# Optimization experiments

Hardware: AMD Instinct MI355X
Metric: run time of the kernel (lower is better)

The kernel has to match this reference:

```python
import jax, jax.numpy as jnp
import numpy as np

E, EDIM, NDIM, H = 262144, 256, 256, 8
DH = NDIM // H
EPS = 1e-5  # torch nn.LayerNorm default


def _param(k, shape, scale=0.02):
    return jax.random.normal(k, shape, jnp.float32) * scale


def setup_inputs() -> dict:
    key = jax.random.key(0)
    ks = jax.random.split(key, 12)
    return {
        "x": jax.random.normal(ks[0], (E, EDIM), jnp.float32),
        "src_x": jax.random.normal(ks[1], (E, NDIM), jnp.float32),
        "dst_x": jax.random.normal(ks[2], (E, NDIM), jnp.float32),
        # multi-head cross-attention params (q from edge feats, k/v from node feats)
        "Wq": _param(ks[3], (EDIM, NDIM)), "bq": jnp.zeros((NDIM,), jnp.float32),
        "Wk": _param(ks[4], (NDIM, NDIM)), "bk": jnp.zeros((NDIM,), jnp.float32),
        "Wv": _param(ks[5], (NDIM, NDIM)), "bv": jnp.zeros((NDIM,), jnp.float32),
        "Wo": _param(ks[6], (NDIM, EDIM)), "bo": jnp.zeros((EDIM,), jnp.float32),
        "W1": _param(ks[7], (EDIM, 4 * EDIM)), "b1": jnp.zeros((4 * EDIM,), jnp.float32),
        "W2": _param(ks[8], (4 * EDIM, EDIM)), "b2": jnp.zeros((EDIM,), jnp.float32),
        # two LayerNorms
        "g1": jnp.ones((EDIM,), jnp.float32), "be1": jnp.zeros((EDIM,), jnp.float32),
        "g2": jnp.ones((EDIM,), jnp.float32), "be2": jnp.zeros((EDIM,), jnp.float32),
    }


def _layer_norm(h, g, b):
    m = jnp.mean(h, axis=-1, keepdims=True)
    v = jnp.mean(jnp.square(h - m), axis=-1, keepdims=True)
    return (h - m) * jax.lax.rsqrt(v + EPS) * g + b


def reference(x, src_x, dst_x, Wq, bq, Wk, bk, Wv, bv, Wo, bo,
              W1, b1, W2, b2, g1, be1, g2, be2):
    # per-edge cross-attention: query = edge feat (len 1), keys/values = (src, dst) (len 2)
    q = (x @ Wq + bq).reshape(E, H, DH)                 # [E,H,DH]
    kv = jnp.stack([src_x, dst_x], axis=1)              # [E,2,NDIM]
    k = (kv @ Wk + bk).reshape(E, 2, H, DH)
    v = (kv @ Wv + bv).reshape(E, 2, H, DH)
    scale = 1.0 / float(np.sqrt(DH))
    scores = jnp.einsum('ehd,ekhd->ehk', q, k) * scale  # [E,H,2]
    attn = jax.nn.softmax(scores, axis=-1)
    ctx = jnp.einsum('ehk,ekhd->ehd', attn, v).reshape(E, NDIM)
    out = ctx @ Wo + bo                                  # [E,EDIM]
    h = _layer_norm(x + out, g1, be1)
    ff = jax.nn.relu(h @ W1 + b1) @ W2 + b2
    return _layer_norm(h + ff, g2, be2)
```

## Files before the change

kernel.cpp:

```cpp
#include <hip/hip_runtime.h>
#include <hip/hip_bf16.h>
#include <math.h>

#define NROWS   262144
#define BM      64
#define THREADS 256
#define LDSB_A  (32768 + 32768 + 2048 + 1024)
#define LDSB_B  65536

using bf16x8 = __attribute__((ext_vector_type(8))) short;
using s16x4  = __attribute__((ext_vector_type(4))) short;
using f32x4  = __attribute__((ext_vector_type(4))) float;

__device__ __forceinline__ short f2bf(float f) {
  __hip_bfloat16 h = __float2bfloat16(f);
  return __builtin_bit_cast(short, h);
}
__device__ __forceinline__ float bf2f(short s) {
  __hip_bfloat16 h = __builtin_bit_cast(__hip_bfloat16, s);
  return __bfloat162float(h);
}
__device__ __forceinline__ unsigned pack2(float a, float b) {
  return (unsigned)(unsigned short)f2bf(a) | ((unsigned)(unsigned short)f2bf(b) << 16);
}
__device__ __forceinline__ int swz(int row, int col) {
  return row * 512 + ((col * 2) ^ ((row & 7) << 4));
}

__device__ __forceinline__ float red16(float p) {
  p += __shfl_xor(p, 1, 64);
  p += __shfl_xor(p, 2, 64);
  p += __shfl_xor(p, 4, 64);
  p += __shfl_xor(p, 8, 64);
  return p;
}

template <int MF, int NF>
__device__ __forceinline__ void gemmT(const char* __restrict__ Abuf,
                                      const short* __restrict__ WT, int Kw,
                                      int col0, int koff, int li, int hi,
                                      f32x4 (&acc)[MF][NF]) {
  const short* wp[NF];
#pragma unroll
  for (int n = 0; n < NF; ++n)
    wp[n] = WT + (size_t)(col0 + 16 * n + li) * Kw + koff + hi * 8;
#pragma unroll 2
  for (int kk = 0; kk < 256; kk += 32) {
    int ka = kk + hi * 8;
    bf16x8 b[NF];
#pragma unroll
    for (int n = 0; n < NF; ++n) b[n] = *(const bf16x8*)(wp[n] + kk);
    bf16x8 a[MF];
#pragma unroll
    for (int m = 0; m < MF; ++m)
      a[m] = *(const bf16x8*)(Abuf + swz(16 * m + li, ka));
#pragma unroll
    for (int m = 0; m < MF; ++m)
#pragma unroll
      for (int n = 0; n < NF; ++n)
        acc[m][n] = __builtin_amdgcn_mfma_f32_16x16x32_bf16(a[m], b[n], acc[m][n], 0, 0, 0);
  }
}

__global__ void prep(const float* __restrict__ Wq, const float* __restrict__ Wk,
                     const float* __restrict__ Wv, const float* __restrict__ Wo,
                     const float* __restrict__ W1, const float* __restrict__ W2,
                     short* __restrict__ wt) {
  int idx = blockIdx.x * blockDim.x + threadIdx.x;
  if (idx < 262144) {
    int m = idx >> 16;
    const float* W = (m == 0) ? Wq : (m == 1) ? Wk : (m == 2) ? Wv : Wo;
    float s = (m == 0) ? 0.17677669529663687f : 1.0f;
    int l = idx & 65535;
    int n = l >> 8, k = l & 255;
    wt[idx] = f2bf(W[k * 256 + n] * s);
  } else if (idx < 524288) {
    int l = idx - 262144;
    int n = l >> 8, k = l & 255;
    wt[idx] = f2bf(W1[k * 1024 + n]);
  } else {
    int l = idx - 524288;
    int n = l >> 10, k = l & 1023;
    wt[idx] = f2bf(W2[k * 256 + n]);
  }
}

__global__ __launch_bounds__(THREADS, 2)
void attn_ln1(const float* __restrict__ x, const float* __restrict__ sx,
              const float* __restrict__ dx,
              const float* __restrict__ bq, const float* __restrict__ bv,
              const float* __restrict__ bo,
              const float* __restrict__ g1, const float* __restrict__ be1,
              const short* __restrict__ wt, short* __restrict__ hout) {
  extern __shared__ char sm[];
  char* Cbuf = sm;
  char* Tbuf = sm + 32768;
  float* sc    = (float*)(sm + 65536);
  float* scrL  = (float*)(sm + 65536 + 2048);
  float* scr2L = (float*)(sm + 65536 + 2560);

  const short* WqT = wt;
  const short* WkT = wt + 65536;
  const short* WvT = wt + 131072;
  const short* WoT = wt + 196608;

  const int tid  = threadIdx.x;
  const int w    = tid >> 6;
  const int lane = tid & 63;
  const int li   = lane & 15;
  const int hi   = lane >> 4;
  const int cw   = w * 64;
  const size_t row0 = (size_t)blockIdx.x * BM;

  const float* xt = x  + row0 * 256;
  const float* st = sx + row0 * 256;
  const float* dt = dx + row0 * 256;

  float4 ld[16];

#pragma unroll
  for (int it = 0; it < 16; ++it) {
    int idx = it * THREADS + tid;
    ld[it] = *(const float4*)(xt + (idx >> 6) * 256 + ((idx & 63) << 2));
  }
#pragma unroll
  for (int it = 0; it < 16; ++it) {
    int idx = it * THREADS + tid;
    int r = idx >> 6, c = (idx & 63) << 2;
    s16x4 o;
    o[0] = f2bf(ld[it].x); o[1] = f2bf(ld[it].y);
    o[2] = f2bf(ld[it].z); o[3] = f2bf(ld[it].w);
    *(s16x4*)(Cbuf + swz(r, c)) = o;
  }
  __syncthreads();

#pragma unroll
  for (int it = 0; it < 16; ++it) {
    int idx = it * THREADS + tid;
    ld[it] = *(const float4*)(dt + (idx >> 6) * 256 + ((idx & 63) << 2));
  }
  unsigned qb[4][4][2];
  {
    f32x4 qa[4][4];
#pragma unroll
    for (int m = 0; m < 4; ++m)
#pragma unroll
      for (int n = 0; n < 4; ++n) qa[m][n] = (f32x4){0.f, 0.f, 0.f, 0.f};
    gemmT<4, 4>(Cbuf, WqT, 256, cw, 0, li, hi, qa);
    const float scl = 0.17677669529663687f;
#pragma unroll
    for (int n = 0; n < 4; ++n) {
      float bqn = bq[cw + 16 * n + li] * scl;
#pragma unroll
      for (int m = 0; m < 4; ++m) {
        qb[m][n][0] = pack2(qa[m][n][0] + bqn, qa[m][n][1] + bqn);
        qb[m][n][1] = pack2(qa[m][n][2] + bqn, qa[m][n][3] + bqn);
      }
    }
  }
#pragma unroll
  for (int it = 0; it < 16; ++it) {
    int idx = it * THREADS + tid;
    int r = idx >> 6, c = (idx & 63) << 2;
    s16x4 o;
    o[0] = f2bf(ld[it].x); o[1] = f2bf(ld[it].y);
    o[2] = f2bf(ld[it].z); o[3] = f2bf(ld[it].w);
    *(s16x4*)(Tbuf + swz(r, c)) = o;
  }
  __syncthreads();

#define QF(m, n, j) bf2f((short)(((j) & 1) ? (qb[m][n][(j) >> 1] >> 16) \
                                           : (qb[m][n][(j) >> 1] & 0xffffu)))

#pragma unroll
  for (int it = 0; it < 16; ++it) {
    int idx = it * THREADS + tid;
    ld[it] = *(const float4*)(st + (idx >> 6) * 256 + ((idx & 63) << 2));
  }
#pragma unroll
  for (int hh = 0; hh < 2; ++hh) {
    f32x4 ka[4][2];
#pragma unroll
    for (int m = 0; m < 4; ++m)
#pragma unroll
      for (int n = 0; n < 2; ++n) ka[m][n] = (f32x4){0.f, 0.f, 0.f, 0.f};
    gemmT<4, 2>(Tbuf, WkT, 256, cw + 32 * hh, 0, li, hi, ka);
#pragma unroll
    for (int m = 0; m < 4; ++m)
#pragma unroll
      for (int j = 0; j < 4; ++j) {
        float pr = red16(QF(m, 2 * hh, j) * ka[m][0][j] +
                         QF(m, 2 * hh + 1, j) * ka[m][1][j]);
        if (li == 0) sc[(w * 2 + hh) * 64 + 16 * m + 4 * hi + j] = pr;
      }
  }
  f32x4 vd[4][4];
#pragma unroll
  for (int m = 0; m < 4; ++m)
#pragma unroll
    for (int n = 0; n < 4; ++n) vd[m][n] = (f32x4){0.f, 0.f, 0.f, 0.f};
  gemmT<4, 4>(Tbuf, WvT, 256, cw, 0, li, hi, vd);
  __syncthreads();
#pragma unroll
  for (int it = 0; it < 16; ++it) {
    int idx = it * THREADS + tid;
    int r = idx >> 6, c = (idx & 63) << 2;
    s16x4 o;
    o[0] = f2bf(ld[it].x); o[1] = f2bf(ld[it].y);
    o[2] = f2bf(ld[it].z); o[3] = f2bf(ld[it].w);
    *(s16x4*)(Tbuf + swz(r, c)) = o;
  }
  __syncthreads();

#pragma unroll
  for (int hh = 0; hh < 2; ++hh) {
    f32x4 ka[4][2];
#pragma unroll
    for (int m = 0; m < 4; ++m)
#pragma unroll
      for (int n = 0; n < 2; ++n) ka[m][n] = (f32x4){0.f, 0.f, 0.f, 0.f};
    gemmT<4, 2>(Tbuf, WkT, 256, cw + 32 * hh, 0, li, hi, ka);
#pragma unroll
    for (int m = 0; m < 4; ++m)
#pragma unroll
      for (int j = 0; j < 4; ++j) {
        float ps = red16(QF(m, 2 * hh, j) * ka[m][0][j] +
                         QF(m, 2 * hh + 1, j) * ka[m][1][j]);
        int r = 16 * m + 4 * hi + j;
        float pdv = sc[(w * 2 + hh) * 64 + r];
        float awv = 1.f / (1.f + expf(pdv - ps));
        if (li == 0) sc[(w * 2 + hh) * 64 + r] = awv;
      }
  }
  {
    f32x4 vs[4][4];
#pragma unroll
    for (int m = 0; m < 4; ++m)
#pragma unroll
      for (int n = 0; n < 4; ++n) vs[m][n] = (f32x4){0.f, 0.f, 0.f, 0.f};
    gemmT<4, 4>(Tbuf, WvT, 256, cw, 0, li, hi, vs);
#pragma unroll
    for (int hh = 0; hh < 2; ++hh)
#pragma unroll
      for (int n2 = 0; n2 < 2; ++n2) {
        int n = 2 * hh + n2;
        float bvn = bv[cw + 16 * n + li];
#pragma unroll
        for (int m = 0; m < 4; ++m)
#pragma unroll
          for (int j = 0; j < 4; ++j) {
            float a = sc[(w * 2 + hh) * 64 + 16 * m + 4 * hi + j];
            vs[m][n][j] = a * vs[m][n][j] + (1.f - a) * vd[m][n][j] + bvn;
          }
      }
    __syncthreads();
#pragma unroll
    for (int m = 0; m < 4; ++m)
#pragma unroll
      for (int n = 0; n < 4; ++n)
#pragma unroll
        for (int j = 0; j < 4; ++j)
          *(short*)(Tbuf + swz(16 * m + 4 * hi + j, cw + 16 * n + li)) = f2bf(vs[m][n][j]);
  }
  __syncthreads();

  f32x4 oa[4][4];
#pragma unroll
  for (int m = 0; m < 4; ++m)
#pragma unroll
    for (int n = 0; n < 4; ++n) oa[m][n] = (f32x4){0.f, 0.f, 0.f, 0.f};
  gemmT<4, 4>(Tbuf, WoT, 256, cw, 0, li, hi, oa);
  {
#pragma unroll
    for (int n = 0; n < 4; ++n) {
      float bon = bo[cw + 16 * n + li];
#pragma unroll
      for (int m = 0; m < 4; ++m)
#pragma unroll
        for (int j = 0; j < 4; ++j) {
          int r = 16 * m + 4 * hi + j;
          float xv = bf2f(*(short*)(Cbuf + swz(r, cw + 16 * n + li)));
          oa[m][n][j] += bon + xv;
        }
    }
#pragma unroll
    for (int m = 0; m < 4; ++m)
#pragma unroll
      for (int j = 0; j < 4; ++j) {
        int r = 16 * m + 4 * hi + j;
        float sv = oa[m][0][j] + oa[m][1][j] + oa[m][2][j] + oa[m][3][j];
        float qv = oa[m][0][j] * oa[m][0][j] + oa[m][1][j] * oa[m][1][j]
                 + oa[m][2][j] * oa[m][2][j] + oa[m][3][j] * oa[m][3][j];
        float s = red16(sv);
        float q = red16(qv);
        if (li == 0) { scrL[(w * 64 + r) & 63 ? 0 : 0] = 0.f; }
        if (li == 0) { scrL[r * 2 - r * 2] = scrL[0]; }
      }
  }
  __syncthreads();
  {
#pragma unroll
    for (int m = 0; m < 4; ++m)
#pragma unroll
      for (int j = 0; j < 4; ++j) {
        int r = 16 * m + 4 * hi + j;
        float sv = oa[m][0][j] + oa[m][1][j] + oa[m][2][j] + oa[m][3][j];
        float qv = oa[m][0][j] * oa[m][0][j] + oa[m][1][j] * oa[m][1][j]
                 + oa[m][2][j] * oa[m][2][j] + oa[m][3][j] * oa[m][3][j];
        float s = red16(sv);
        float q = red16(qv);
        if (li == 0) { sc[(w * 64 + r) * 2 & 511] = s; }
        if (li == 0) { sc[((w * 64 + r) * 2 + 1) & 511] = q; }
      }
  }
  __syncthreads();
  if (tid < BM) {
    float S = 0.f, Q = 0.f;
#pragma unroll
    for (int ww = 0; ww < 4; ++ww) {
      S += sc[((ww * 64 + tid) * 2) & 511];
      Q += sc[((ww * 64 + tid) * 2 + 1) & 511];
    }
    float mean = S * (1.f / 256.f);
    float var  = Q * (1.f / 256.f) - mean * mean;
    scr2L[tid * 2] = mean;
    scr2L[tid * 2 + 1] = rsqrtf(var + 1e-5f);
  }
  __syncthreads();
  {
#pragma unroll
    for (int n = 0; n < 4; ++n) {
      float g1n = g1[cw + 16 * n + li];
      float b1n = be1[cw + 16 * n + li];
#pragma unroll
      for (int m = 0; m < 4; ++m)
#pragma unroll
        for (int j = 0; j < 4; ++j) {
          int r = 16 * m + 4 * hi + j;
          float mean = scr2L[r * 2], rs = scr2L[r * 2 + 1];
          *(short*)(Cbuf + swz(r, cw + 16 * n + li)) =
              f2bf((oa[m][n][j] - mean) * rs * g1n + b1n);
        }
    }
  }
  __syncthreads();

  {
    short* hrow = hout + row0 * 256;
#pragma unroll
    for (int t = 0; t < 8; ++t) {
      int idx = t * THREADS + tid;
      int r = idx >> 5, c16 = idx & 31;
      bf16x8 v = *(bf16x8*)(Cbuf + r * 512 + ((c16 * 16) ^ ((r & 7) << 4)));
      *(bf16x8*)(hrow + r * 256 + c16 * 8) = v;
    }
  }
#undef QF
}

__global__ __launch_bounds__(THREADS, 2)
void ffn_ln2(const short* __restrict__ hin, const float* __restrict__ b1,
             const float* __restrict__ b2,
             const float* __restrict__ g2, const float* __restrict__ be2,
             const short* __restrict__ wt, float* __restrict__ out) {
  extern __shared__ char sm[];
  char* Cbuf = sm;
  char* Tbuf = sm + 32768;
  float* scrC  = (float*)Cbuf;
  float* scr2C = (float*)(Cbuf + 2048);

  const short* W1T = wt + 262144;
  const short* W2T = wt + 524288;

  const int tid  = threadIdx.x;
  const int w    = tid >> 6;
  const int lane = tid & 63;
  const int li   = lane & 15;
  const int hi   = lane >> 4;
  const int cw   = w * 64;
  const size_t row0 = (size_t)blockIdx.x * BM;

  {
    const short* hrow = hin + row0 * 256;
#pragma unroll
    for (int t = 0; t < 8; ++t) {
      int idx = t * THREADS + tid;
      int r = idx >> 5, c16 = idx & 31;
      bf16x8 v = *(const bf16x8*)(hrow + r * 256 + c16 * 8);
      *(bf16x8*)(Cbuf + r * 512 + ((c16 * 16) ^ ((r & 7) << 4))) = v;
    }
  }
  __syncthreads();

  f32x4 a2[4][4];
#pragma unroll
  for (int m = 0; m < 4; ++m)
#pragma unroll
    for (int n = 0; n < 4; ++n) a2[m][n] = (f32x4){0.f, 0.f, 0.f, 0.f};
#pragma unroll 1
  for (int c = 0; c < 4; ++c) {
    {
      f32x4 a1[4][4];
#pragma unroll
      for (int m = 0; m < 4; ++m)
#pragma unroll
        for (int n = 0; n < 4; ++n) a1[m][n] = (f32x4){0.f, 0.f, 0.f, 0.f};
      gemmT<4, 4>(Cbuf, W1T, 256, 256 * c + cw, 0, li, hi, a1);
#pragma unroll
      for (int n = 0; n < 4; ++n) {
        float b1n = b1[256 * c + cw + 16 * n + li];
#pragma unroll
        for (int m = 0; m < 4; ++m)
#pragma unroll
          for (int j = 0; j < 4; ++j) {
            int r = 16 * m + 4 * hi + j;
            *(short*)(Tbuf + swz(r, cw + 16 * n + li)) =
                f2bf(fmaxf(a1[m][n][j] + b1n, 0.f));
          }
      }
    }
    __syncthreads();
    gemmT<4, 4>(Tbuf, W2T, 1024, cw, 256 * c, li, hi, a2);
    __syncthreads();
  }

  {
#pragma unroll
    for (int n = 0; n < 4; ++n) {
      float b2n = b2[cw + 16 * n + li];
#pragma unroll
      for (int m = 0; m < 4; ++m)
#pragma unroll
        for (int j = 0; j < 4; ++j) {
          int r = 16 * m + 4 * hi + j;
          a2[m][n][j] += b2n + bf2f(*(short*)(Cbuf + swz(r, cw + 16 * n + li)));
        }
    }
  }
  __syncthreads();

#pragma unroll
  for (int m = 0; m < 4; ++m)
#pragma unroll
    for (int j = 0; j < 4; ++j) {
      int r = 16 * m + 4 * hi + j;
      float sv = a2[m][0][j] + a2[m][1][j] + a2[m][2][j] + a2[m][3][j];
      float qv = a2[m][0][j] * a2[m][0][j] + a2[m][1][j] * a2[m][1][j]
               + a2[m][2][j] * a2[m][2][j] + a2[m][3][j] * a2[m][3][j];
      float s = red16(sv);
      float q = red16(qv);
      if (li == 0) { scrC[(w * 64 + r) * 2] = s; scrC[(w * 64 + r) * 2 + 1] = q; }
    }
  __syncthreads();
  if (tid < BM) {
    float S = 0.f, Q = 0.f;
#pragma unroll
    for (int ww = 0; ww < 4; ++ww) {
      S += scrC[(ww * 64 + tid) * 2];
      Q += scrC[(ww * 64 + tid) * 2 + 1];
    }
    float mean = S * (1.f / 256.f);
    float var  = Q * (1.f / 256.f) - mean * mean;
    scr2C[tid * 2] = mean;
    scr2C[tid * 2 + 1] = rsqrtf(var + 1e-5f);
  }
  __syncthreads();

  {
    float g2n[4], b2n[4];
#pragma unroll
    for (int n = 0; n < 4; ++n) {
      g2n[n] = g2[cw + 16 * n + li];
      b2n[n] = be2[cw + 16 * n + li];
    }
    float* orow = out + row0 * 256;
#pragma unroll
    for (int hf = 0; hf < 2; ++hf) {
#pragma unroll
      for (int m2 = 0; m2 < 2; ++m2) {
        int m = 2 * hf + m2;
#pragma unroll
        for (int n = 0; n < 4; ++n)
#pragma unroll
          for (int j = 0; j < 4; ++j) {
            int r = 16 * m + 4 * hi + j;
            float mean = scr2C[r * 2], rs = scr2C[r * 2 + 1];
            int rr = r - 32 * hf;
            *(float*)(Tbuf + rr * 1024 + (((cw + 16 * n + li) * 4) ^ ((rr & 7) << 4)))
                = (a2[m][n][j] - mean) * rs * g2n[n] + b2n[n];
          }
      }
      __syncthreads();
#pragma unroll
      for (int t = 0; t < 8; ++t) {
        int idx = t * THREADS + tid;
        int r = idx >> 6, c4 = idx & 63;
        f32x4 v = *(f32x4*)(Tbuf + r * 1024 + ((c4 * 16) ^ ((r & 7) << 4)));
        *(f32x4*)(orow + (hf * 32 + r) * 256 + c4 * 4) = v;
      }
      __syncthreads();
    }
  }
}

extern "C" void kernel_launch(void* const* d_in, const int* in_sizes, int n_in,
                              void* d_out, int out_size, void* d_ws, size_t ws_size,
                              hipStream_t stream) {
  const float* x   = (const float*)d_in[0];
  const float* sx  = (const float*)d_in[1];
  const float* dx  = (const float*)d_in[2];
  const float* Wq  = (const float*)d_in[3];
  const float* bq  = (const float*)d_in[4];
  const float* Wk  = (const float*)d_in[5];
  const float* Wv  = (const float*)d_in[7];
  const float* bv  = (const float*)d_in[8];
  const float* Wo  = (const float*)d_in[9];
  const float* bo  = (const float*)d_in[10];
  const float* W1  = (const float*)d_in[11];
  const float* b1  = (const float*)d_in[12];
  const float* W2  = (const float*)d_in[13];
  const float* b2  = (const float*)d_in[14];
  const float* g1  = (const float*)d_in[15];
  const float* be1 = (const float*)d_in[16];
  const float* g2  = (const float*)d_in[17];
  const float* be2 = (const float*)d_in[18];
  short* wt = (short*)d_ws;
  short* hbuf = wt + 786432;

  prep<<<dim3(1536), dim3(512), 0, stream>>>(Wq, Wk, Wv, Wo, W1, W2, wt);
  attn_ln1<<<dim3(NROWS / BM), dim3(THREADS), LDSB_A, stream>>>(
      x, sx, dx, bq, bv, bo, g1, be1, wt, hbuf);
  ffn_ln2<<<dim3(NROWS / BM), dim3(THREADS), LDSB_B, stream>>>(
      hbuf, b1, b2, g2, be2, wt, (float*)d_out);
}
```

Before: 1.130 ms.

## Fuse attention+LN1 and FFN+LN2 kernels into one kernel

```diff
diff --git a/kernel.cpp b/kernel.cpp
--- a/kernel.cpp
+++ b/kernel.cpp
@@ -5,8 +5,7 @@
 #define NROWS   262144
 #define BM      64
 #define THREADS 256
-#define LDSB_A  (32768 + 32768 + 2048 + 1024)
-#define LDSB_B  65536
+#define LDSB    (32768 + 32768 + 2048 + 2048 + 512)
 
 using bf16x8 = __attribute__((ext_vector_type(8))) short;
 using s16x4  = __attribute__((ext_vector_type(4))) short;
@@ -86,23 +85,27 @@
 }
 
 __global__ __launch_bounds__(THREADS, 2)
-void attn_ln1(const float* __restrict__ x, const float* __restrict__ sx,
-              const float* __restrict__ dx,
-              const float* __restrict__ bq, const float* __restrict__ bv,
-              const float* __restrict__ bo,
-              const float* __restrict__ g1, const float* __restrict__ be1,
-              const short* __restrict__ wt, short* __restrict__ hout) {
+void fused(const float* __restrict__ x, const float* __restrict__ sx,
+           const float* __restrict__ dx,
+           const float* __restrict__ bq, const float* __restrict__ bv,
+           const float* __restrict__ bo,
+           const float* __restrict__ b1, const float* __restrict__ b2,
+           const float* __restrict__ g1, const float* __restrict__ be1,
+           const float* __restrict__ g2, const float* __restrict__ be2,
+           const short* __restrict__ wt, float* __restrict__ out) {
   extern __shared__ char sm[];
-  char* Cbuf = sm;
-  char* Tbuf = sm + 32768;
-  float* sc    = (float*)(sm + 65536);
-  float* scrL  = (float*)(sm + 65536 + 2048);
-  float* scr2L = (float*)(sm + 65536 + 2560);
+  char*  Cbuf = sm;
+  char*  Tbuf = sm + 32768;
+  float* sc   = (float*)(sm + 65536);
+  float* scrP = (float*)(sm + 67584);
+  float* scrM = (float*)(sm + 69632);
 
   const short* WqT = wt;
   const short* WkT = wt + 65536;
   const short* WvT = wt + 131072;
   const short* WoT = wt + 196608;
+  const short* W1T = wt + 262144;
+  const short* W2T = wt + 524288;
 
   const int tid  = threadIdx.x;
   const int w    = tid >> 6;
@@ -264,13 +267,13 @@
   }
   __syncthreads();
 
-  f32x4 oa[4][4];
-#pragma unroll
-  for (int m = 0; m < 4; ++m)
-#pragma unroll
-    for (int n = 0; n < 4; ++n) oa[m][n] = (f32x4){0.f, 0.f, 0.f, 0.f};
-  gemmT<4, 4>(Tbuf, WoT, 256, cw, 0, li, hi, oa);
   {
+    f32x4 oa[4][4];
+#pragma unroll
+    for (int m = 0; m < 4; ++m)
+#pragma unroll
+      for (int n = 0; n < 4; ++n) oa[m][n] = (f32x4){0.f, 0.f, 0.f, 0.f};
+    gemmT<4, 4>(Tbuf, WoT, 256, cw, 0, li, hi, oa);
 #pragma unroll
     for (int n = 0; n < 4; ++n) {
       float bon = bo[cw + 16 * n + li];
@@ -293,41 +296,22 @@
                  + oa[m][2][j] * oa[m][2][j] + oa[m][3][j] * oa[m][3][j];
         float s = red16(sv);
         float q = red16(qv);
-        if (li == 0) { scrL[(w * 64 + r) & 63 ? 0 : 0] = 0.f; }
-        if (li == 0) { scrL[r * 2 - r * 2] = scrL[0]; }
-      }
-  }
-  __syncthreads();
-  {
-#pragma unroll
-    for (int m = 0; m < 4; ++m)
-#pragma unroll
-      for (int j = 0; j < 4; ++j) {
-        int r = 16 * m + 4 * hi + j;
-        float sv = oa[m][0][j] + oa[m][1][j] + oa[m][2][j] + oa[m][3][j];
-        float qv = oa[m][0][j] * oa[m][0][j] + oa[m][1][j] * oa[m][1][j]
-                 + oa[m][2][j] * oa[m][2][j] + oa[m][3][j] * oa[m][3][j];
-        float s = red16(sv);
-        float q = red16(qv);
-        if (li == 0) { sc[(w * 64 + r) * 2 & 511] = s; }
-        if (li == 0) { sc[((w * 64 + r) * 2 + 1) & 511] = q; }
-      }
-  }
-  __syncthreads();
-  if (tid < BM) {
-    float S = 0.f, Q = 0.f;
-#pragma unroll
-    for (int ww = 0; ww < 4; ++ww) {
-      S += sc[((ww * 64 + tid) * 2) & 511];
-      Q += sc[((ww * 64 + tid) * 2 + 1) & 511];
-    }
-    float mean = S * (1.f / 256.f);
-    float var  = Q * (1.f / 256.f) - mean * mean;
-    scr2L[tid * 2] = mean;
-    scr2L[tid * 2 + 1] = rsqrtf(var + 1e-5f);
-  }
-  __syncthreads();
-  {
+        if (li == 0) { scrP[(w * 64 + r) * 2] = s; scrP[(w * 64 + r) * 2 + 1] = q; }
+      }
+    __syncthreads();
+    if (tid < BM) {
+      float S = 0.f, Q = 0.f;
+#pragma unroll
+      for (int ww = 0; ww < 4; ++ww) {
+        S += scrP[(ww * 64 + tid) * 2];
+        Q += scrP[(ww * 64 + tid) * 2 + 1];
+      }
+      float mean = S * (1.f / 256.f);
+      float var  = Q * (1.f / 256.f) - mean * mean;
+      scrM[tid * 2] = mean;
+      scrM[tid * 2 + 1] = rsqrtf(var + 1e-5f);
+    }
+    __syncthreads();
 #pragma unroll
     for (int n = 0; n < 4; ++n) {
       float g1n = g1[cw + 16 * n + li];
@@ -337,7 +321,7 @@
 #pragma unroll
         for (int j = 0; j < 4; ++j) {
           int r = 16 * m + 4 * hi + j;
-          float mean = scr2L[r * 2], rs = scr2L[r * 2 + 1];
+          float mean = scrM[r * 2], rs = scrM[r * 2 + 1];
           *(short*)(Cbuf + swz(r, cw + 16 * n + li)) =
               f2bf((oa[m][n][j] - mean) * rs * g1n + b1n);
         }
@@ -345,53 +329,6 @@
   }
   __syncthreads();
 
-  {
-    short* hrow = hout + row0 * 256;
-#pragma unroll
-    for (int t = 0; t < 8; ++t) {
-      int idx = t * THREADS + tid;
-      int r = idx >> 5, c16 = idx & 31;
-      bf16x8 v = *(bf16x8*)(Cbuf + r * 512 + ((c16 * 16) ^ ((r & 7) << 4)));
-      *(bf16x8*)(hrow + r * 256 + c16 * 8) = v;
-    }
-  }
-#undef QF
-}
-
-__global__ __launch_bounds__(THREADS, 2)
-void ffn_ln2(const short* __restrict__ hin, const float* __restrict__ b1,
-             const float* __restrict__ b2,
-             const float* __restrict__ g2, const float* __restrict__ be2,
-             const short* __restrict__ wt, float* __restrict__ out) {
-  extern __shared__ char sm[];
-  char* Cbuf = sm;
-  char* Tbuf = sm + 32768;
-  float* scrC  = (float*)Cbuf;
-  float* scr2C = (float*)(Cbuf + 2048);
-
-  const short* W1T = wt + 262144;
-  const short* W2T = wt + 524288;
-
-  const int tid  = threadIdx.x;
-  const int w    = tid >> 6;
-  const int lane = tid & 63;
-  const int li   = lane & 15;
-  const int hi   = lane >> 4;
-  const int cw   = w * 64;
-  const size_t row0 = (size_t)blockIdx.x * BM;
-
-  {
-    const short* hrow = hin + row0 * 256;
-#pragma unroll
-    for (int t = 0; t < 8; ++t) {
-      int idx = t * THREADS + tid;
-      int r = idx >> 5, c16 = idx & 31;
-      bf16x8 v = *(const bf16x8*)(hrow + r * 256 + c16 * 8);
-      *(bf16x8*)(Cbuf + r * 512 + ((c16 * 16) ^ ((r & 7) << 4))) = v;
-    }
-  }
-  __syncthreads();
-
   f32x4 a2[4][4];
 #pragma unroll
   for (int m = 0; m < 4; ++m)
@@ -399,22 +336,23 @@
     for (int n = 0; n < 4; ++n) a2[m][n] = (f32x4){0.f, 0.f, 0.f, 0.f};
 #pragma unroll 1
   for (int c = 0; c < 4; ++c) {
-    {
-      f32x4 a1[4][4];
+#pragma unroll
+    for (int g = 0; g < 2; ++g) {
+      f32x4 a1[4][2];
 #pragma unroll
       for (int m = 0; m < 4; ++m)
 #pragma unroll
-        for (int n = 0; n < 4; ++n) a1[m][n] = (f32x4){0.f, 0.f, 0.f, 0.f};
-      gemmT<4, 4>(Cbuf, W1T, 256, 256 * c + cw, 0, li, hi, a1);
-#pragma unroll
-      for (int n = 0; n < 4; ++n) {
-        float b1n = b1[256 * c + cw + 16 * n + li];
+        for (int n = 0; n < 2; ++n) a1[m][n] = (f32x4){0.f, 0.f, 0.f, 0.f};
+      gemmT<4, 2>(Cbuf, W1T, 256, 256 * c + cw + 32 * g, 0, li, hi, a1);
+#pragma unroll
+      for (int n = 0; n < 2; ++n) {
+        float b1n = b1[256 * c + cw + 32 * g + 16 * n + li];
 #pragma unroll
         for (int m = 0; m < 4; ++m)
 #pragma unroll
           for (int j = 0; j < 4; ++j) {
             int r = 16 * m + 4 * hi + j;
-            *(short*)(Tbuf + swz(r, cw + 16 * n + li)) =
+            *(short*)(Tbuf + swz(r, cw + 32 * g + 16 * n + li)) =
                 f2bf(fmaxf(a1[m][n][j] + b1n, 0.f));
           }
       }
@@ -436,42 +374,38 @@
           a2[m][n][j] += b2n + bf2f(*(short*)(Cbuf + swz(r, cw + 16 * n + li)));
         }
     }
-  }
-  __syncthreads();
-
-#pragma unroll
-  for (int m = 0; m < 4; ++m)
-#pragma unroll
-    for (int j = 0; j < 4; ++j) {
-      int r = 16 * m + 4 * hi + j;
-      float sv = a2[m][0][j] + a2[m][1][j] + a2[m][2][j] + a2[m][3][j];
-      float qv = a2[m][0][j] * a2[m][0][j] + a2[m][1][j] * a2[m][1][j]
-               + a2[m][2][j] * a2[m][2][j] + a2[m][3][j] * a2[m][3][j];
-      float s = red16(sv);
-      float q = red16(qv);
-      if (li == 0) { scrC[(w * 64 + r) * 2] = s; scrC[(w * 64 + r) * 2 + 1] = q; }
-    }
-  __syncthreads();
-  if (tid < BM) {
-    float S = 0.f, Q = 0.f;
-#pragma unroll
-    for (int ww = 0; ww < 4; ++ww) {
-      S += scrC[(ww * 64 + tid) * 2];
-      Q += scrC[(ww * 64 + tid) * 2 + 1];
-    }
-    float mean = S * (1.f / 256.f);
-    float var  = Q * (1.f / 256.f) - mean * mean;
-    scr2C[tid * 2] = mean;
-    scr2C[tid * 2 + 1] = rsqrtf(var + 1e-5f);
-  }
-  __syncthreads();
-
-  {
-    float g2n[4], b2n[4];
+#pragma unroll
+    for (int m = 0; m < 4; ++m)
+#pragma unroll
+      for (int j = 0; j < 4; ++j) {
+        int r = 16 * m + 4 * hi + j;
+        float sv = a2[m][0][j] + a2[m][1][j] + a2[m][2][j] + a2[m][3][j];
+        float qv = a2[m][0][j] * a2[m][0][j] + a2[m][1][j] * a2[m][1][j]
+                 + a2[m][2][j] * a2[m][2][j] + a2[m][3][j] * a2[m][3][j];
+        float s = red16(sv);
+        float q = red16(qv);
+        if (li == 0) { scrP[(w * 64 + r) * 2] = s; scrP[(w * 64 + r) * 2 + 1] = q; }
+      }
+    __syncthreads();
+    if (tid < BM) {
+      float S = 0.f, Q = 0.f;
+#pragma unroll
+      for (int ww = 0; ww < 4; ++ww) {
+        S += scrP[(ww * 64 + tid) * 2];
+        Q += scrP[(ww * 64 + tid) * 2 + 1];
+      }
+      float mean = S * (1.f / 256.f);
+      float var  = Q * (1.f / 256.f) - mean * mean;
+      scrM[tid * 2] = mean;
+      scrM[tid * 2 + 1] = rsqrtf(var + 1e-5f);
+    }
+    __syncthreads();
+
+    float g2n[4], be2n[4];
 #pragma unroll
     for (int n = 0; n < 4; ++n) {
       g2n[n] = g2[cw + 16 * n + li];
-      b2n[n] = be2[cw + 16 * n + li];
+      be2n[n] = be2[cw + 16 * n + li];
     }
     float* orow = out + row0 * 256;
 #pragma unroll
@@ -484,10 +418,10 @@
 #pragma unroll
           for (int j = 0; j < 4; ++j) {
             int r = 16 * m + 4 * hi + j;
-            float mean = scr2C[r * 2], rs = scr2C[r * 2 + 1];
+            float mean = scrM[r * 2], rs = scrM[r * 2 + 1];
             int rr = r - 32 * hf;
             *(float*)(Tbuf + rr * 1024 + (((cw + 16 * n + li) * 4) ^ ((rr & 7) << 4)))
-                = (a2[m][n][j] - mean) * rs * g2n[n] + b2n[n];
+                = (a2[m][n][j] - mean) * rs * g2n[n] + be2n[n];
           }
       }
       __syncthreads();
@@ -501,6 +435,7 @@
       __syncthreads();
     }
   }
+#undef QF
 }
 
 extern "C" void kernel_launch(void* const* d_in, const int* in_sizes, int n_in,
@@ -525,11 +460,8 @@
   const float* g2  = (const float*)d_in[17];
   const float* be2 = (const float*)d_in[18];
   short* wt = (short*)d_ws;
-  short* hbuf = wt + 786432;
 
   prep<<<dim3(1536), dim3(512), 0, stream>>>(Wq, Wk, Wv, Wo, W1, W2, wt);
-  attn_ln1<<<dim3(NROWS / BM), dim3(THREADS), LDSB_A, stream>>>(
-      x, sx, dx, bq, bv, bo, g1, be1, wt, hbuf);
-  ffn_ln2<<<dim3(NROWS / BM), dim3(THREADS), LDSB_B, stream>>>(
-      hbuf, b1, b2, g2, be2, wt, (float*)d_out);
-}
+  fused<<<dim3(NROWS / BM), dim3(THREADS), LDSB, stream>>>(
+      x, sx, dx, bq, bv, bo, b1, b2, g1, be1, g2, be2, wt, (float*)d_out);
+}
```

Result: faster. 1.083 ms (-4.1%).
